# Kernel optimization log

Hardware: AMD Instinct MI355X
Metric: run time of the kernel (lower is better)

The kernel has to match this reference:

```python
import jax, jax.numpy as jnp
import numpy as np
from jax import lax


def _dense_image_warp(img, flow):
    # TFA semantics: out[b,i,j] = bilinear_sample(img[b], (i - flow[b,i,j,0], j - flow[b,i,j,1]))
    # floors clamped to [0, size-2]; alphas clamped to [0, 1].
    B, H, W, C = img.shape
    gy = jnp.arange(H, dtype=flow.dtype)[None, :, None]
    gx = jnp.arange(W, dtype=flow.dtype)[None, None, :]
    qy = gy - flow[..., 0]
    qx = gx - flow[..., 1]
    fy = jnp.clip(jnp.floor(qy), 0.0, H - 2)
    fx = jnp.clip(jnp.floor(qx), 0.0, W - 2)
    ay = jnp.clip(qy - fy, 0.0, 1.0)[..., None]
    ax = jnp.clip(qx - fx, 0.0, 1.0)[..., None]
    fy = fy.astype(jnp.int32)
    fx = fx.astype(jnp.int32)
    b = jnp.arange(B)[:, None, None]
    tl = img[b, fy, fx]
    tr = img[b, fy, fx + 1]
    bl = img[b, fy + 1, fx]
    br = img[b, fy + 1, fx + 1]
    top = tl + ax * (tr - tl)
    bot = bl + ax * (br - bl)
    return top + ay * (bot - top)


def _conv(x, w, b, act):
    y = lax.conv_general_dilated(x, w, (1, 1), 'SAME',
                                 dimension_numbers=('NHWC', 'HWIO', 'NHWC')) + b
    return jax.nn.relu(y) if act else y


def _predict(x, ws, bs):
    for i in range(4):
        x = _conv(x, ws[i], bs[i], True)
    return _conv(x, ws[4], bs[4], False)  # final 1x1 -> 2 channels, linear


def _upsample2x(x):
    B, H, W, C = x.shape
    return jax.image.resize(x, (B, 2 * H, 2 * W, C), method='bilinear')


# Conv stack dims: in=64 (concat of two 32-ch maps)
_KSHAPES = [(3, 3, 64, 32), (3, 3, 32, 64), (1, 1, 64, 64), (1, 1, 64, 16), (1, 1, 16, 2)]


def setup_inputs() -> dict:
    key = jax.random.key(0)
    ks = jax.random.split(key, 4 + 2 * len(_KSHAPES))
    B, H, W, C = 8, 256, 256, 32
    inp = {
        'input_1': jax.random.normal(ks[0], (B, H, W, C), jnp.float32),
        'input_2': jax.random.normal(ks[1], (B, H, W, C), jnp.float32),
        'flow_1_2': jax.random.normal(ks[2], (B, H, W, 2), jnp.float32) * 3.0,
        'flow_2_1': jax.random.normal(ks[3], (B, H, W, 2), jnp.float32) * 3.0,
    }
    for i, sh in enumerate(_KSHAPES):
        inp[f'w12_{i}'] = jax.random.normal(ks[4 + i], sh, jnp.float32) * 0.05
        inp[f'b12_{i}'] = jnp.zeros((sh[-1],), jnp.float32)
        inp[f'w21_{i}'] = jax.random.normal(ks[4 + len(_KSHAPES) + i], sh, jnp.float32) * 0.05
        inp[f'b21_{i}'] = jnp.zeros((sh[-1],), jnp.float32)
    return inp


def reference(input_1, input_2, flow_1_2, flow_2_1,
              w12_0, b12_0, w12_1, b12_1, w12_2, b12_2, w12_3, b12_3, w12_4, b12_4,
              w21_0, b21_0, w21_1, b21_1, w21_2, b21_2, w21_3, b21_3, w21_4, b21_4):
    ws12 = [w12_0, w12_1, w12_2, w12_3, w12_4]
    bs12 = [b12_0, b12_1, b12_2, b12_3, b12_4]
    ws21 = [w21_0, w21_1, w21_2, w21_3, w21_4]
    bs21 = [b21_0, b21_1, b21_2, b21_3, b21_4]

    # 1 -> 2 direction
    input_1_warped_1 = _dense_image_warp(input_1, flow_1_2)
    flow_change_1_2 = _predict(jnp.concatenate([input_2, input_1_warped_1], axis=3), ws12, bs12)
    flow_1_2_changed = flow_1_2 + flow_change_1_2
    input_1_warped_2 = _dense_image_warp(input_1, flow_1_2_changed)
    flow_1_2_up = _upsample2x(flow_1_2_changed)

    # 2 -> 1 direction
    input_2_warped_1 = _dense_image_warp(input_2, flow_2_1)
    flow_change_2_1 = _predict(jnp.concatenate([input_1, input_2_warped_1], axis=3), ws21, bs21)
    flow_2_1_changed = flow_2_1 + flow_change_2_1
    input_2_warped_2 = _dense_image_warp(input_2, flow_2_1_changed)
    flow_2_1_up = _upsample2x(flow_2_1_changed)

    return (input_1_warped_2, input_2_warped_2, flow_1_2_up, flow_2_1_up)
```

## Files before the change

kernel.cpp:

```cpp
#include <hip/hip_runtime.h>
#include <hip/hip_bf16.h>
#include <cstddef>

#define B_ 8
#define H_ 256
#define W_ 256

static constexpr int NPIX = B_ * H_ * W_;

typedef __attribute__((ext_vector_type(8))) short bf16x8;
typedef __attribute__((ext_vector_type(4))) float f32x4;

__device__ __forceinline__ float4 ld4(const float* p) { return *(const float4*)p; }

__device__ __forceinline__ short f2bf(float x) {
    unsigned u = __float_as_uint(x);
    unsigned r = (u + 0x7fffu + ((u >> 16) & 1u)) >> 16;
    return (short)r;
}

__device__ __forceinline__ void warp_bf16_body(
    int gid, const float* __restrict__ in1, const float* __restrict__ in2,
    const float* __restrict__ fl12, const float* __restrict__ fl21,
    short* __restrict__ wbf)
{
    int d   = (gid >= NPIX * 8);
    int g2  = gid - (d ? NPIX * 8 : 0);
    const float* img  = d ? in2 : in1;
    const float* flow = d ? fl21 : fl12;
    short* out = wbf + (size_t)d * NPIX * 32;

    int p   = g2 >> 3;
    int c4  = (g2 & 7) << 2;
    int b   = p >> 16;
    int i   = (p >> 8) & 255;
    int j   = p & 255;
    float2 f = *(const float2*)(flow + (size_t)p * 2);
    float qy = (float)i - f.x;
    float qx = (float)j - f.y;
    float fyf = fminf(fmaxf(floorf(qy), 0.0f), (float)(H_ - 2));
    float fxf = fminf(fmaxf(floorf(qx), 0.0f), (float)(W_ - 2));
    float ay = fminf(fmaxf(qy - fyf, 0.0f), 1.0f);
    float ax = fminf(fmaxf(qx - fxf, 0.0f), 1.0f);
    int fy = (int)fyf, fx = (int)fxf;
    const float* base = img + ((((size_t)b * H_ + fy) * W_ + fx) << 5) + c4;
    float4 tl = ld4(base);
    float4 tr = ld4(base + 32);
    float4 bl = ld4(base + W_ * 32);
    float4 br = ld4(base + W_ * 32 + 32);
    short4 r;
    { float t = tl.x + ax * (tr.x - tl.x); float u = bl.x + ax * (br.x - bl.x); r.x = f2bf(t + ay * (u - t)); }
    { float t = tl.y + ax * (tr.y - tl.y); float u = bl.y + ax * (br.y - bl.y); r.y = f2bf(t + ay * (u - t)); }
    { float t = tl.z + ax * (tr.z - tl.z); float u = bl.z + ax * (br.z - bl.z); r.z = f2bf(t + ay * (u - t)); }
    { float t = tl.w + ax * (tr.w - tl.w); float u = bl.w + ax * (br.w - bl.w); r.w = f2bf(t + ay * (u - t)); }
    *(short4*)(out + ((size_t)p << 5) + c4) = r;
}

__device__ __forceinline__ void cvt_body(
    int t, const float* __restrict__ in1, const float* __restrict__ in2,
    short* __restrict__ xb1, short* __restrict__ xb2)
{
    const int N8 = NPIX * 32 / 8;
    const float* src = (t < N8) ? in1 : in2;
    short* dst = (t < N8) ? xb1 : xb2;
    int i = (t < N8) ? t : t - N8;
    float4 a = ld4(src + (size_t)i * 8);
    float4 b = ld4(src + (size_t)i * 8 + 4);
    bf16x8 r;
    r[0] = f2bf(a.x); r[1] = f2bf(a.y); r[2] = f2bf(a.z); r[3] = f2bf(a.w);
    r[4] = f2bf(b.x); r[5] = f2bf(b.y); r[6] = f2bf(b.z); r[7] = f2bf(b.w);
    *(bf16x8*)(dst + (size_t)i * 8) = r;
}

__device__ __forceinline__ void prep_body(
    int t,
    const float* __restrict__ w0a, const float* __restrict__ w1a,
    const float* __restrict__ w2a, const float* __restrict__ w3a,
    const float* __restrict__ w0b, const float* __restrict__ w1b,
    const float* __restrict__ w2b, const float* __restrict__ w3b,
    short* __restrict__ wt0, short* __restrict__ wt1)
{
    if (t >= 2 * 5248) return;
    int dir = t / 5248;
    int r = t % 5248;
    const float* w0 = dir ? w0b : w0a;
    const float* w1 = dir ? w1b : w1a;
    const float* w2 = dir ? w2b : w2a;
    const float* w3 = dir ? w3b : w3a;
    short* wt = dir ? wt1 : wt0;
    bf16x8 v;
    if (r < 2304) {
        int l = r & 63, n = (r >> 6) & 1, c = (r >> 7) & 1, tp = r >> 8;
#pragma unroll
        for (int j = 0; j < 8; ++j) {
            int ci = c * 32 + 8 * (l >> 4) + j;
            int co = n * 16 + (l & 15);
            v[j] = f2bf(w0[(size_t)(tp * 64 + ci) * 32 + co]);
        }
    } else if (r < 4608) {
        int q = r - 2304;
        int l = q & 63, n = (q >> 6) & 3, tp = q >> 8;
#pragma unroll
        for (int j = 0; j < 8; ++j) {
            int ci = 8 * (l >> 4) + j;
            int co = n * 16 + (l & 15);
            v[j] = f2bf(w1[(size_t)(tp * 32 + ci) * 64 + co]);
        }
    } else if (r < 5120) {
        int q = r - 4608;
        int l = q & 63, n = (q >> 6) & 3, c = q >> 8;
#pragma unroll
        for (int j = 0; j < 8; ++j) {
            int k = 32 * c + 8 * (l >> 4) + j;
            int co = n * 16 + (l & 15);
            v[j] = f2bf(w2[(size_t)k * 64 + co]);
        }
    } else {
        int q = r - 5120;
        int l = q & 63, c = q >> 6;
#pragma unroll
        for (int j = 0; j < 8; ++j) {
            int k = 32 * c + 8 * (l >> 4) + j;
            v[j] = f2bf(w3[(size_t)k * 16 + (l & 15)]);
        }
    }
    *(bf16x8*)(wt + (size_t)r * 8) = v;
}

__global__ __launch_bounds__(256) void pre_kernel(
    const float* __restrict__ in1, const float* __restrict__ in2,
    const float* __restrict__ fl12, const float* __restrict__ fl21,
    short* __restrict__ xb1, short* __restrict__ xb2, short* __restrict__ wbf,
    const float* __restrict__ w0a, const float* __restrict__ w1a,
    const float* __restrict__ w2a, const float* __restrict__ w3a,
    const float* __restrict__ w0b, const float* __restrict__ w1b,
    const float* __restrict__ w2b, const float* __restrict__ w3b,
    short* __restrict__ wt0, short* __restrict__ wt1)
{
    const int NW = 2 * NPIX * 8 / 256;
    const int NC = NPIX * 64 / 8 / 256;
    int blk = blockIdx.x;
    if (blk < NW) {
        warp_bf16_body(blk * 256 + threadIdx.x, in1, in2, fl12, fl21, wbf);
    } else if (blk < NW + NC) {
        cvt_body((blk - NW) * 256 + threadIdx.x, in1, in2, xb1, xb2);
    } else {
        prep_body((blk - NW - NC) * 256 + threadIdx.x,
                  w0a, w1a, w2a, w3a, w0b, w1b, w2b, w3b, wt0, wt1);
    }
}

__device__ __forceinline__ int xcd_swz(int orig) {
    return (orig & 7) * 512 + (orig >> 3);
}

__global__ __launch_bounds__(512) void conv0_mfma_kernel(
    const short* __restrict__ xb1, const short* __restrict__ xb2,
    const short* __restrict__ wbf,
    const short* __restrict__ wt0, const short* __restrict__ wt1,
    const float* __restrict__ b0a, const float* __restrict__ b0b,
    short* __restrict__ h0)
{
    __shared__ short swt[2304 * 8];
    int wg  = xcd_swz(blockIdx.x);
    int d   = wg >> 11;
    int bid = wg & 2047;
    const short* xoth = d ? xb1 : xb2;
    const short* xw   = wbf + (size_t)d * NPIX * 32;
    const short* wtab = d ? wt1 : wt0;
    const float* bias = d ? b0b : b0a;
    short* out = h0 + (size_t)d * NPIX * 32;

    int tid = threadIdx.x;
    for (int i = tid; i < 2304; i += 512)
        ((bf16x8*)swt)[i] = ((const bf16x8*)wtab)[i];
    __syncthreads();

    int wave = tid >> 6, lane = tid & 63;
    int l15 = lane & 15, g = lane >> 4;
    int prow = bid * 256;
    int y    = bid & 255;
    int t0   = prow + wave * 32;
    int xl0  = wave * 32 + l15;
    int xl1  = xl0 + 16;

    const short* a0p = xoth + ((size_t)(t0 + l15) << 5) + g * 8;
    const short* a1p = a0p + (16 << 5);
    const short* b0p = xw + ((size_t)(t0 + l15) << 5) + g * 8;
    const short* b1p = b0p + (16 << 5);
    const bf16x8* wfrag = (const bf16x8*)swt;

    float bv0 = bias[l15], bv1 = bias[16 + l15];
    f32x4 acc00 = {bv0, bv0, bv0, bv0};
    f32x4 acc01 = {bv1, bv1, bv1, bv1};
    f32x4 acc10 = {bv0, bv0, bv0, bv0};
    f32x4 acc11 = {bv1, bv1, bv1, bv1};
    const bf16x8 z8 = {0, 0, 0, 0, 0, 0, 0, 0};

#pragma unroll
    for (int dy = -1; dy <= 1; ++dy) {
        if ((unsigned)(y + dy) >= (unsigned)H_) continue;
#pragma unroll
        for (int dx = -1; dx <= 1; ++dx) {
            bool v0 = (unsigned)(xl0 + dx) < (unsigned)W_;
            bool v1 = (unsigned)(xl1 + dx) < (unsigned)W_;
            int off0 = (dy * W_ + (v0 ? dx : 0)) << 5;
            int off1 = (dy * W_ + (v1 ? dx : 0)) << 5;
            bf16x8 aA0 = *(const bf16x8*)(a0p + off0);
            bf16x8 aB0 = *(const bf16x8*)(b0p + off0);
            bf16x8 aA1 = *(const bf16x8*)(a1p + off1);
            bf16x8 aB1 = *(const bf16x8*)(b1p + off1);
            aA0 = v0 ? aA0 : z8;  aB0 = v0 ? aB0 : z8;
            aA1 = v1 ? aA1 : z8;  aB1 = v1 ? aB1 : z8;
            int t = (dy + 1) * 3 + (dx + 1);
            bf16x8 w0 = wfrag[(t * 4 + 0) * 64 + lane];
            bf16x8 w1 = wfrag[(t * 4 + 1) * 64 + lane];
            bf16x8 w2 = wfrag[(t * 4 + 2) * 64 + lane];
            bf16x8 w3 = wfrag[(t * 4 + 3) * 64 + lane];
            acc00 = __builtin_amdgcn_mfma_f32_16x16x32_bf16(aA0, w0, acc00, 0, 0, 0);
            acc01 = __builtin_amdgcn_mfma_f32_16x16x32_bf16(aA0, w1, acc01, 0, 0, 0);
            acc10 = __builtin_amdgcn_mfma_f32_16x16x32_bf16(aA1, w0, acc10, 0, 0, 0);
            acc11 = __builtin_amdgcn_mfma_f32_16x16x32_bf16(aA1, w1, acc11, 0, 0, 0);
            acc00 = __builtin_amdgcn_mfma_f32_16x16x32_bf16(aB0, w2, acc00, 0, 0, 0);
            acc01 = __builtin_amdgcn_mfma_f32_16x16x32_bf16(aB0, w3, acc01, 0, 0, 0);
            acc10 = __builtin_amdgcn_mfma_f32_16x16x32_bf16(aB1, w2, acc10, 0, 0, 0);
            acc11 = __builtin_amdgcn_mfma_f32_16x16x32_bf16(aB1, w3, acc11, 0, 0, 0);
        }
    }

#pragma unroll
    for (int r = 0; r < 4; ++r) {
        size_t r0 = (size_t)(t0 + g * 4 + r) << 5;
        size_t r1 = (size_t)(t0 + 16 + g * 4 + r) << 5;
        out[r0 + l15]      = f2bf(fmaxf(acc00[r], 0.f));
        out[r0 + 16 + l15] = f2bf(fmaxf(acc01[r], 0.f));
        out[r1 + l15]      = f2bf(fmaxf(acc10[r], 0.f));
        out[r1 + 16 + l15] = f2bf(fmaxf(acc11[r], 0.f));
    }
}

__global__ __launch_bounds__(512) void conv1_mfma_kernel(
    const short* __restrict__ h0,
    const short* __restrict__ wt0, const short* __restrict__ wt1,
    const float* __restrict__ b1a, const float* __restrict__ b1b,
    const float* __restrict__ b2a, const float* __restrict__ b2b,
    const float* __restrict__ b3a, const float* __restrict__ b3b,
    const float* __restrict__ w4a, const float* __restrict__ w4b,
    const float* __restrict__ b4a, const float* __restrict__ b4b,
    const float* __restrict__ fl12, const float* __restrict__ fl21,
    float* __restrict__ fcb)
{
    __shared__ short swt[2944 * 8];
    __shared__ __align__(16) short sx[8][2048];
    int wg  = xcd_swz(blockIdx.x);
    int d   = wg >> 11;
    int bid = wg & 2047;
    const short* hsrc = h0 + (size_t)d * NPIX * 32;
    const short* wtab = (d ? wt1 : wt0) + 2304 * 8;
    const float* b1 = d ? b1b : b1a;
    const float* b2 = d ? b2b : b2a;
    const float* b3 = d ? b3b : b3a;
    const float* w4 = d ? w4b : w4a;
    const float* b4 = d ? b4b : b4a;
    const float* flow = d ? fl21 : fl12;
    float* fc = fcb + (size_t)d * NPIX * 2;

    int tid = threadIdx.x;
    for (int i = tid; i < 2944; i += 512)
        ((bf16x8*)swt)[i] = ((const bf16x8*)wtab)[i];
    __syncthreads();

    int wave = tid >> 6, lane = tid & 63;
    int l15 = lane & 15, g = lane >> 4;
    int prow = bid * 256;
    int y    = bid & 255;
    int t0   = prow + wave * 32;
    int xl0  = wave * 32 + l15;
    int xl1  = xl0 + 16;

    const short* a0p = hsrc + ((size_t)(t0 + l15) << 5) + g * 8;
    const short* a1p = a0p + (16 << 5);
    const bf16x8* W1 = (const bf16x8*)swt;
    const bf16x8* W2 = (const bf16x8*)swt + 2304;
    const bf16x8* W3 = (const bf16x8*)swt + 2816;
    char* xb = (char*)&sx[wave][0];
    const bf16x8 z8 = {0, 0, 0, 0, 0, 0, 0, 0};

    f32x4 acc0[4], acc1[4];
#pragma unroll
    for (int n = 0; n < 4; ++n) {
        float b = b1[n * 16 + l15];
        acc0[n] = (f32x4){b, b, b, b};
        acc1[n] = (f32x4){b, b, b, b};
    }
#pragma unroll
    for (int dy = -1; dy <= 1; ++dy) {
        if ((unsigned)(y + dy) >= (unsigned)H_) continue;
#pragma unroll
        for (int dx = -1; dx <= 1; ++dx) {
            bool v0 = (unsigned)(xl0 + dx) < (unsigned)W_;
            bool v1 = (unsigned)(xl1 + dx) < (unsigned)W_;
            int off0 = (dy * W_ + (v0 ? dx : 0)) << 5;
            int off1 = (dy * W_ + (v1 ? dx : 0)) << 5;
            bf16x8 a0 = *(const bf16x8*)(a0p + off0);
            bf16x8 a1 = *(const bf16x8*)(a1p + off1);
            a0 = v0 ? a0 : z8;
            a1 = v1 ? a1 : z8;
            int t = (dy + 1) * 3 + (dx + 1);
#pragma unroll
            for (int n = 0; n < 4; ++n) {
                bf16x8 w = W1[(t * 4 + n) * 64 + lane];
                acc0[n] = __builtin_amdgcn_mfma_f32_16x16x32_bf16(a0, w, acc0[n], 0, 0, 0);
                acc1[n] = __builtin_amdgcn_mfma_f32_16x16x32_bf16(a1, w, acc1[n], 0, 0, 0);
            }
        }
    }
#pragma unroll
    for (int n = 0; n < 4; ++n)
#pragma unroll
        for (int r = 0; r < 4; ++r) {
            int row0 = g * 4 + r, ch = n * 16 + l15;
            int by0 = (row0 * 128 + ch * 2) ^ ((row0 & 7) << 4);
            int by1 = ((row0 + 16) * 128 + ch * 2) ^ ((row0 & 7) << 4);
            *(short*)(xb + by0) = f2bf(fmaxf(acc0[n][r], 0.f));
            *(short*)(xb + by1) = f2bf(fmaxf(acc1[n][r], 0.f));
        }

#pragma unroll
    for (int n = 0; n < 4; ++n) {
        float b = b2[n * 16 + l15];
        acc0[n] = (f32x4){b, b, b, b};
        acc1[n] = (f32x4){b, b, b, b};
    }
#pragma unroll
    for (int c = 0; c < 2; ++c) {
        int by0 = (l15 * 128 + (32 * c + 8 * g) * 2) ^ ((l15 & 7) << 4);
        int by1 = ((l15 + 16) * 128 + (32 * c + 8 * g) * 2) ^ ((l15 & 7) << 4);
        bf16x8 a0 = *(const bf16x8*)(xb + by0);
        bf16x8 a1 = *(const bf16x8*)(xb + by1);
#pragma unroll
        for (int n = 0; n < 4; ++n) {
            bf16x8 w = W2[(c * 4 + n) * 64 + lane];
            acc0[n] = __builtin_amdgcn_mfma_f32_16x16x32_bf16(a0, w, acc0[n], 0, 0, 0);
            acc1[n] = __builtin_amdgcn_mfma_f32_16x16x32_bf16(a1, w, acc1[n], 0, 0, 0);
        }
    }
#pragma unroll
    for (int n = 0; n < 4; ++n)
#pragma unroll
        for (int r = 0; r < 4; ++r) {
            int row0 = g * 4 + r, ch = n * 16 + l15;
            int by0 = (row0 * 128 + ch * 2) ^ ((row0 & 7) << 4);
            int by1 = ((row0 + 16) * 128 + ch * 2) ^ ((row0 & 7) << 4);
            *(short*)(xb + by0) = f2bf(fmaxf(acc0[n][r], 0.f));
            *(short*)(xb + by1) = f2bf(fmaxf(acc1[n][r], 0.f));
        }

    float b3v = b3[l15];
    f32x4 acc3a = {b3v, b3v, b3v, b3v};
    f32x4 acc3b = {b3v, b3v, b3v, b3v};
#pragma unroll
    for (int c = 0; c < 2; ++c) {
        int by0 = (l15 * 128 + (32 * c + 8 * g) * 2) ^ ((l15 & 7) << 4);
        int by1 = ((l15 + 16) * 128 + (32 * c + 8 * g) * 2) ^ ((l15 & 7) << 4);
        bf16x8 a0 = *(const bf16x8*)(xb + by0);
        bf16x8 a1 = *(const bf16x8*)(xb + by1);
        bf16x8 w = W3[c * 64 + lane];
        acc3a = __builtin_amdgcn_mfma_f32_16x16x32_bf16(a0, w, acc3a, 0, 0, 0);
        acc3b = __builtin_amdgcn_mfma_f32_16x16x32_bf16(a1, w, acc3b, 0, 0, 0);
    }

    float w40 = w4[l15 * 2 + 0], w41 = w4[l15 * 2 + 1];
    float bb0 = b4[0], bb1 = b4[1];
#pragma unroll
    for (int tt = 0; tt < 2; ++tt) {
        f32x4 a3 = tt ? acc3b : acc3a;
#pragma unroll
        for (int r = 0; r < 4; ++r) {
            float v = fmaxf(a3[r], 0.f);
            float s0 = v * w40, s1 = v * w41;
#pragma unroll
            for (int m = 1; m < 16; m <<= 1) {
                s0 += __shfl_xor(s0, m);
                s1 += __shfl_xor(s1, m);
            }
            if (l15 == 0) {
                int pr = t0 + tt * 16 + g * 4 + r;
                float2 fl = *(const float2*)(flow + (size_t)pr * 2);
                float2 o; o.x = fl.x + bb0 + s0; o.y = fl.y + bb1 + s1;
                *(float2*)(fc + (size_t)pr * 2) = o;
            }
        }
    }
}

__device__ __forceinline__ void warp_f32_body(
    int gid, const float* __restrict__ in1, const float* __restrict__ in2,
    const float* __restrict__ fcb, float* __restrict__ outf)
{
    int d   = (gid >= NPIX * 8);
    int g2  = gid - (d ? NPIX * 8 : 0);
    const float* img  = d ? in2 : in1;
    const float* flow = fcb + (size_t)d * NPIX * 2;
    float* out = outf + (size_t)d * NPIX * 32;

    int p   = g2 >> 3;
    int c4  = (g2 & 7) << 2;
    int b   = p >> 16;
    int i   = (p >> 8) & 255;
    int j   = p & 255;
    float2 f = *(const float2*)(flow + (size_t)p * 2);
    float qy = (float)i - f.x;
    float qx = (float)j - f.y;
    float fyf = fminf(fmaxf(floorf(qy), 0.0f), (float)(H_ - 2));
    float fxf = fminf(fmaxf(floorf(qx), 0.0f), (float)(W_ - 2));
    float ay = fminf(fmaxf(qy - fyf, 0.0f), 1.0f);
    float ax = fminf(fmaxf(qx - fxf, 0.0f), 1.0f);
    int fy = (int)fyf, fx = (int)fxf;
    const float* base = img + ((((size_t)b * H_ + fy) * W_ + fx) << 5) + c4;
    float4 tl = ld4(base);
    float4 tr = ld4(base + 32);
    float4 bl = ld4(base + W_ * 32);
    float4 br = ld4(base + W_ * 32 + 32);
    float4 r;
    { float t = tl.x + ax * (tr.x - tl.x); float u = bl.x + ax * (br.x - bl.x); r.x = t + ay * (u - t); }
    { float t = tl.y + ax * (tr.y - tl.y); float u = bl.y + ax * (br.y - bl.y); r.y = t + ay * (u - t); }
    { float t = tl.z + ax * (tr.z - tl.z); float u = bl.z + ax * (br.z - bl.z); r.z = t + ay * (u - t); }
    { float t = tl.w + ax * (tr.w - tl.w); float u = bl.w + ax * (br.w - bl.w); r.w = t + ay * (u - t); }
    *(float4*)(out + ((size_t)p << 5) + c4) = r;
}

__device__ __forceinline__ void upsample_body(
    int gid, const float* __restrict__ fcb, float* __restrict__ outup)
{
    const int NUP = B_ * 512 * 512;
    int d  = (gid >= NUP);
    int g2 = gid - (d ? NUP : 0);
    const float* fc = fcb + (size_t)d * NPIX * 2;
    float* out = outup + (size_t)d * NUP * 2;

    int b  = g2 >> 18;
    int oy = (g2 >> 9) & 511;
    int ox = g2 & 511;
    float iy = 0.5f * (float)oy - 0.25f;
    float ix = 0.5f * (float)ox - 0.25f;
    float y0f = floorf(iy), x0f = floorf(ix);
    float wy = iy - y0f, wx = ix - x0f;
    int y0 = min(max((int)y0f, 0), H_ - 1);
    int y1 = min(max((int)y0f + 1, 0), H_ - 1);
    int x0 = min(max((int)x0f, 0), W_ - 1);
    int x1 = min(max((int)x0f + 1, 0), W_ - 1);
    float2 v00 = *(const float2*)(fc + (((size_t)b * H_ + y0) * W_ + x0) * 2);
    float2 v01 = *(const float2*)(fc + (((size_t)b * H_ + y0) * W_ + x1) * 2);
    float2 v10 = *(const float2*)(fc + (((size_t)b * H_ + y1) * W_ + x0) * 2);
    float2 v11 = *(const float2*)(fc + (((size_t)b * H_ + y1) * W_ + x1) * 2);
    float2 r;
    { float t = v00.x + wx * (v01.x - v00.x); float u = v10.x + wx * (v11.x - v10.x); r.x = t + wy * (u - t); }
    { float t = v00.y + wx * (v01.y - v00.y); float u = v10.y + wx * (v11.y - v10.y); r.y = t + wy * (u - t); }
    *(float2*)(out + (size_t)g2 * 2) = r;
}

__global__ __launch_bounds__(256) void post_kernel(
    const float* __restrict__ in1, const float* __restrict__ in2,
    const float* __restrict__ fcb, float* __restrict__ outf,
    float* __restrict__ outup)
{
    const int NWF = 2 * NPIX * 8 / 256;
    int blk = blockIdx.x;
    if (blk < NWF) {
        warp_f32_body(blk * 256 + threadIdx.x, in1, in2, fcb, outf);
    } else {
        upsample_body((blk - NWF) * 256 + threadIdx.x, fcb, outup);
    }
}

extern "C" void kernel_launch(void* const* d_in, const int* in_sizes, int n_in,
                              void* d_out, int out_size, void* d_ws, size_t ws_size,
                              hipStream_t stream)
{
    (void)in_sizes; (void)n_in; (void)out_size; (void)ws_size;
    const float* input1 = (const float*)d_in[0];
    const float* input2 = (const float*)d_in[1];
    const float* fl12 = (const float*)d_in[2];
    const float* fl21 = (const float*)d_in[3];
    char* wsb = (char*)d_ws;
    short* xb1  = (short*)(wsb);
    short* xb2  = (short*)(wsb + 33554432);
    short* wbf  = (short*)(wsb + 67108864);
    short* h0   = (short*)(wsb + 134217728);
    float* fcb  = (float*)(wsb + 201326592);
    short* wt0  = (short*)(wsb + 209715200);
    short* wt1  = (short*)(wsb + 209715200 + 5248 * 16);
    float* outf = (float*)d_out;
    float* outup = outf + (size_t)2 * NPIX * 32;

    const int NPRE = 2 * NPIX * 8 / 256 + NPIX * 64 / 8 / 256 + (2 * 5248 + 255) / 256;
    pre_kernel<<<NPRE, 256, 0, stream>>>(
        input1, input2, fl12, fl21, xb1, xb2, wbf,
        (const float*)d_in[4],  (const float*)d_in[8],  (const float*)d_in[12], (const float*)d_in[16],
        (const float*)d_in[6],  (const float*)d_in[10], (const float*)d_in[14], (const float*)d_in[18],
        wt0, wt1);
    conv0_mfma_kernel<<<2 * NPIX / 256, 512, 0, stream>>>(
        xb1, xb2, wbf, wt0, wt1,
        (const float*)d_in[5], (const float*)d_in[7], h0);
    conv1_mfma_kernel<<<2 * NPIX / 256, 512, 0, stream>>>(
        h0, wt0, wt1,
        (const float*)d_in[9],  (const float*)d_in[11],
        (const float*)d_in[13], (const float*)d_in[15],
        (const float*)d_in[17], (const float*)d_in[19],
        (const float*)d_in[20], (const float*)d_in[22],
        (const float*)d_in[21], (const float*)d_in[23],
        fl12, fl21, fcb);
    const int NPOST = 2 * NPIX * 8 / 256 + 2 * B_ * 512 * 512 / 256;
    post_kernel<<<NPOST, 256, 0, stream>>>(input1, input2, fcb, outf, outup);
}
```

Before: 581.1 us.

## Shrink conv1 LDS footprint by streaming 1x1 weights from global and halving scratch

The conv1 kernel no longer stages the 1x1 layer weights (W2/W3) in shared memory; they are read directly from global memory instead. The per-wave scratch buffer is halved by running the 1x1 tail for each 16-pixel half separately through a lambda. Launch bounds now request 6 blocks per CU. The aim is less LDS and register use so more workgroups fit per CU, at the cost of extra global/L2 weight loads and a serialized tail per half.

```diff
diff --git a/kernel.cpp b/kernel.cpp
--- a/kernel.cpp
+++ b/kernel.cpp
@@ -239,7 +239,7 @@
     }
 }
 
-__global__ __launch_bounds__(512) void conv1_mfma_kernel(
+__global__ __launch_bounds__(512, 6) void conv1_mfma_kernel(
     const short* __restrict__ h0,
     const short* __restrict__ wt0, const short* __restrict__ wt1,
     const float* __restrict__ b1a, const float* __restrict__ b1b,
@@ -250,8 +250,8 @@
     const float* __restrict__ fl12, const float* __restrict__ fl21,
     float* __restrict__ fcb)
 {
-    __shared__ short swt[2944 * 8];
-    __shared__ __align__(16) short sx[8][2048];
+    __shared__ short swt[2304 * 8];
+    __shared__ __align__(16) short sx[8][1024];
     int wg  = xcd_swz(blockIdx.x);
     int d   = wg >> 11;
     int bid = wg & 2047;
@@ -266,7 +266,7 @@
     float* fc = fcb + (size_t)d * NPIX * 2;
 
     int tid = threadIdx.x;
-    for (int i = tid; i < 2944; i += 512)
+    for (int i = tid; i < 2304; i += 512)
         ((bf16x8*)swt)[i] = ((const bf16x8*)wtab)[i];
     __syncthreads();
 
@@ -281,8 +281,6 @@
     const short* a0p = hsrc + ((size_t)(t0 + l15) << 5) + g * 8;
     const short* a1p = a0p + (16 << 5);
     const bf16x8* W1 = (const bf16x8*)swt;
-    const bf16x8* W2 = (const bf16x8*)swt + 2304;
-    const bf16x8* W3 = (const bf16x8*)swt + 2816;
     char* xb = (char*)&sx[wave][0];
     const bf16x8 z8 = {0, 0, 0, 0, 0, 0, 0, 0};
 
@@ -315,66 +313,53 @@
             }
         }
     }
-#pragma unroll
-    for (int n = 0; n < 4; ++n)
-#pragma unroll
-        for (int r = 0; r < 4; ++r) {
-            int row0 = g * 4 + r, ch = n * 16 + l15;
-            int by0 = (row0 * 128 + ch * 2) ^ ((row0 & 7) << 4);
-            int by1 = ((row0 + 16) * 128 + ch * 2) ^ ((row0 & 7) << 4);
-            *(short*)(xb + by0) = f2bf(fmaxf(acc0[n][r], 0.f));
-            *(short*)(xb + by1) = f2bf(fmaxf(acc1[n][r], 0.f));
-        }
-
-#pragma unroll
-    for (int n = 0; n < 4; ++n) {
-        float b = b2[n * 16 + l15];
-        acc0[n] = (f32x4){b, b, b, b};
-        acc1[n] = (f32x4){b, b, b, b};
-    }
-#pragma unroll
-    for (int c = 0; c < 2; ++c) {
-        int by0 = (l15 * 128 + (32 * c + 8 * g) * 2) ^ ((l15 & 7) << 4);
-        int by1 = ((l15 + 16) * 128 + (32 * c + 8 * g) * 2) ^ ((l15 & 7) << 4);
-        bf16x8 a0 = *(const bf16x8*)(xb + by0);
-        bf16x8 a1 = *(const bf16x8*)(xb + by1);
-#pragma unroll
-        for (int n = 0; n < 4; ++n) {
-            bf16x8 w = W2[(c * 4 + n) * 64 + lane];
-            acc0[n] = __builtin_amdgcn_mfma_f32_16x16x32_bf16(a0, w, acc0[n], 0, 0, 0);
-            acc1[n] = __builtin_amdgcn_mfma_f32_16x16x32_bf16(a1, w, acc1[n], 0, 0, 0);
-        }
-    }
-#pragma unroll
-    for (int n = 0; n < 4; ++n)
-#pragma unroll
-        for (int r = 0; r < 4; ++r) {
-            int row0 = g * 4 + r, ch = n * 16 + l15;
-            int by0 = (row0 * 128 + ch * 2) ^ ((row0 & 7) << 4);
-            int by1 = ((row0 + 16) * 128 + ch * 2) ^ ((row0 & 7) << 4);
-            *(short*)(xb + by0) = f2bf(fmaxf(acc0[n][r], 0.f));
-            *(short*)(xb + by1) = f2bf(fmaxf(acc1[n][r], 0.f));
-        }
 
     float b3v = b3[l15];
-    f32x4 acc3a = {b3v, b3v, b3v, b3v};
-    f32x4 acc3b = {b3v, b3v, b3v, b3v};
-#pragma unroll
-    for (int c = 0; c < 2; ++c) {
-        int by0 = (l15 * 128 + (32 * c + 8 * g) * 2) ^ ((l15 & 7) << 4);
-        int by1 = ((l15 + 16) * 128 + (32 * c + 8 * g) * 2) ^ ((l15 & 7) << 4);
-        bf16x8 a0 = *(const bf16x8*)(xb + by0);
-        bf16x8 a1 = *(const bf16x8*)(xb + by1);
-        bf16x8 w = W3[c * 64 + lane];
-        acc3a = __builtin_amdgcn_mfma_f32_16x16x32_bf16(a0, w, acc3a, 0, 0, 0);
-        acc3b = __builtin_amdgcn_mfma_f32_16x16x32_bf16(a1, w, acc3b, 0, 0, 0);
-    }
-
     float w40 = w4[l15 * 2 + 0], w41 = w4[l15 * 2 + 1];
     float bb0 = b4[0], bb1 = b4[1];
-#pragma unroll
-    for (int tt = 0; tt < 2; ++tt) {
-        f32x4 a3 = tt ? acc3b : acc3a;
+    float b2v[4];
+#pragma unroll
+    for (int n = 0; n < 4; ++n) b2v[n] = b2[n * 16 + l15];
+
+    const short* w23 = (const short*)((const bf16x8*)wtab + 2304);
+
+    auto tail = [&](f32x4 (&accT)[4], int tbase, const short* wb) {
+        const bf16x8* W2 = (const bf16x8*)wb;
+        const bf16x8* W3 = (const bf16x8*)wb + 512;
+#pragma unroll
+        for (int n = 0; n < 4; ++n)
+#pragma unroll
+            for (int r = 0; r < 4; ++r) {
+                int row = g * 4 + r, ch = n * 16 + l15;
+                int by = (row * 128 + ch * 2) ^ ((row & 7) << 4);
+                *(short*)(xb + by) = f2bf(fmaxf(accT[n][r], 0.f));
+            }
+        f32x4 t2[4];
+#pragma unroll
+        for (int n = 0; n < 4; ++n) t2[n] = (f32x4){b2v[n], b2v[n], b2v[n], b2v[n]};
+#pragma unroll
+        for (int c = 0; c < 2; ++c) {
+            int by = (l15 * 128 + (32 * c + 8 * g) * 2) ^ ((l15 & 7) << 4);
+            bf16x8 a = *(const bf16x8*)(xb + by);
+#pragma unroll
+            for (int n = 0; n < 4; ++n)
+                t2[n] = __builtin_amdgcn_mfma_f32_16x16x32_bf16(a, W2[(c * 4 + n) * 64 + lane], t2[n], 0, 0, 0);
+        }
+#pragma unroll
+        for (int n = 0; n < 4; ++n)
+#pragma unroll
+            for (int r = 0; r < 4; ++r) {
+                int row = g * 4 + r, ch = n * 16 + l15;
+                int by = (row * 128 + ch * 2) ^ ((row & 7) << 4);
+                *(short*)(xb + by) = f2bf(fmaxf(t2[n][r], 0.f));
+            }
+        f32x4 a3 = {b3v, b3v, b3v, b3v};
+#pragma unroll
+        for (int c = 0; c < 2; ++c) {
+            int by = (l15 * 128 + (32 * c + 8 * g) * 2) ^ ((l15 & 7) << 4);
+            bf16x8 a = *(const bf16x8*)(xb + by);
+            a3 = __builtin_amdgcn_mfma_f32_16x16x32_bf16(a, W3[c * 64 + lane], a3, 0, 0, 0);
+        }
 #pragma unroll
         for (int r = 0; r < 4; ++r) {
             float v = fmaxf(a3[r], 0.f);
@@ -385,13 +370,17 @@
                 s1 += __shfl_xor(s1, m);
             }
             if (l15 == 0) {
-                int pr = t0 + tt * 16 + g * 4 + r;
+                int pr = tbase + g * 4 + r;
                 float2 fl = *(const float2*)(flow + (size_t)pr * 2);
                 float2 o; o.x = fl.x + bb0 + s0; o.y = fl.y + bb1 + s1;
                 *(float2*)(fc + (size_t)pr * 2) = o;
             }
         }
-    }
+    };
+    asm volatile("" : "+v"(w23));
+    tail(acc0, t0, w23);
+    asm volatile("" : "+v"(w23));
+    tail(acc1, t0 + 16, w23);
 }
 
 __device__ __forceinline__ void warp_f32_body(
```

New measurement: 660.9 us. 13.7% more time.
